# Performance work log

Measured on AMD Instinct MI355X. Metric: run time of the kernel, lower is better.

## Reference

```python
import jax, jax.numpy as jnp
import numpy as np

PAD = 32
NCLS = 33  # background + 32 instances
EPS = 1e-6


def lovasz_hinge_flat(logits, labels):
    # logits, labels: flat [P]; labels in {0,1} float
    signs = 2.0 * labels - 1.0
    errors = 1.0 - logits * signs
    perm = jnp.argsort(-errors)  # descending
    errors_sorted = errors[perm]
    gt_sorted = labels[perm]
    gts = gt_sorted.sum()
    intersection = gts - jnp.cumsum(gt_sorted)
    union = gts + jnp.cumsum(1.0 - gt_sorted)
    jaccard = 1.0 - intersection / union
    grad = jnp.concatenate([jaccard[:1], jaccard[1:] - jaccard[:-1]])
    return jnp.dot(jax.nn.relu(errors_sorted), jax.lax.stop_gradient(grad))


def setup_inputs() -> dict:
    key = jax.random.key(0)
    k1, k2, k3, k4, k5, k6 = jax.random.split(key, 6)
    B, C, H, W = 2, 16, 192, 192
    return {
        "y_embeddings": jax.random.normal(k1, (B, C, H, W), dtype=jnp.float32),
        "y_true": jax.random.randint(k2, (B, H, W), 0, NCLS),
        "W1": jax.random.normal(k3, (C, 32), dtype=jnp.float32) * 0.25,
        "b1": jax.random.normal(k4, (32,), dtype=jnp.float32) * 0.1,
        "W2": jax.random.normal(k5, (32,), dtype=jnp.float32) * 0.25,
        "b2": jax.random.normal(k6, (1,), dtype=jnp.float32) * 0.1,
    }


def reference(y_embeddings, y_true, W1, b1, W2, b2):
    def per_image(emb, gt):
        # emb: [C,H,W]; gt: [H,W] int
        emb = jnp.pad(emb, ((0, 0), (PAD, PAD), (PAD, PAD)))
        gt = jnp.pad(gt, ((PAD, PAD), (PAD, PAD)))
        # one-hot instance masks (drop background class 0): [N,Hp,Wp]
        oh = jnp.moveaxis(jax.nn.one_hot(gt, NCLS, dtype=emb.dtype), -1, 0)[1:]
        counts = jax.lax.stop_gradient(oh.sum(axis=(1, 2)) + EPS)  # [N]
        centers = jax.lax.stop_gradient(
            jnp.einsum('nhw,chw->nc', oh, emb) / counts[:, None])  # [N,C]
        # broadcast offsets: [N,C,Hp,Wp]
        sims = (centers[:, :, None, None] - emb[None]) / 32.0
        sims = jnp.clip(sims, -2.0, 2.0)
        feats = jnp.moveaxis(sims, 1, -1)  # [N,Hp,Wp,C]
        h = jax.nn.relu(feats @ W1 + b1)  # [N,Hp,Wp,32]
        logits = h @ W2 + b2[0]  # [N,Hp,Wp]
        return lovasz_hinge_flat(logits.reshape(-1), oh.reshape(-1))

    losses = jax.vmap(per_image)(y_embeddings, y_true)
    return jnp.mean(losses)
```

## Files before the change

kernel.cpp:

```cpp
#include <hip/hip_runtime.h>

#define NBINS 1024
#define IMG_HW 36864
#define T 256
#define BLKPI 144
#define NINST 32
#define CCH 16
#define NH 32
#define PADW 28672
#define NB 2
#define EPSF 1e-6f
#define NACC (NINST * (CCH + 1))

typedef unsigned long long u64;
typedef long long i64;
typedef float f32x4 __attribute__((ext_vector_type(4)));

#define OFF_WG   0
#define OFF_CSUM 16384
#define OFF_MAXB 25088
#define OFF_META 26240

__global__ void __launch_bounds__(256)
k_zero(u64* __restrict__ csum, float* __restrict__ out) {
    int tid = threadIdx.x;
    for (int i = tid; i < NB * NACC; i += 256) csum[i] = 0ull;
    if (tid == 0) out[0] = 0.f;
}

__global__ void __launch_bounds__(T)
k_centers(const float* __restrict__ emb, const int* __restrict__ gt,
          u64* __restrict__ csum, float* __restrict__ maxblk,
          u64* __restrict__ wg) {
    int blk = blockIdx.x, b = blockIdx.y;
    int tid = threadIdx.x;
    __shared__ i64 acc[NACC];
    __shared__ float mred[T / 64];

    int pix = blk * T + tid;
    int gtv = gt[(size_t)b * IMG_HW + pix];
    const float* e = emb + (size_t)b * CCH * IMG_HW + pix;
    float ev[CCH];
    float me = 0.f;
#pragma unroll
    for (int c = 0; c < CCH; c++) {
        ev[c] = e[c * IMG_HW];
        me = fmaxf(me, fabsf(ev[c]));
    }

    for (int i = tid; i < NACC; i += T) acc[i] = 0;
    int gid = (b * BLKPI + blk) * T + tid;
    if (gid < NB * NBINS) wg[gid] = 0ull;
    __syncthreads();

    if (gtv > 0) {
        int n = gtv - 1;
#pragma unroll
        for (int c = 0; c < CCH; c++) {
            i64 fx = (i64)((double)ev[c] * 4294967296.0);
            atomicAdd((u64*)&acc[n * CCH + c], (u64)fx);
        }
        atomicAdd((u64*)&acc[NINST * CCH + n], 1ull);
    }
#pragma unroll
    for (int off = 32; off > 0; off >>= 1) me = fmaxf(me, __shfl_down(me, off, 64));
    if ((tid & 63) == 0) mred[tid >> 6] = me;
    __syncthreads();
    if (tid == 0) {
        float m = 0.f;
#pragma unroll
        for (int w = 0; w < T / 64; w++) m = fmaxf(m, mred[w]);
        maxblk[b * BLKPI + blk] = m;
    }
    u64* cb = csum + (size_t)b * NACC;
    for (int i = tid; i < NACC; i += T) {
        u64 v = (u64)acc[i];
        if (v) atomicAdd(&cb[i], v);
    }
}

__global__ void __launch_bounds__(T, 2)
k_hist(const float* __restrict__ emb, const int* __restrict__ gt,
       const float* __restrict__ W1, const float* __restrict__ b1,
       const float* __restrict__ W2, const float* __restrict__ b2,
       const u64* __restrict__ csum, const float* __restrict__ maxblk,
       float* __restrict__ meta, u64* __restrict__ wg) {
    __shared__ unsigned int hist[NBINS];
    __shared__ __align__(16) float q_s[NINST][NH];
    __shared__ float a_s[NINST][CCH];
    __shared__ float redf[T / 64], redm[T / 64];
    __shared__ float semax[NINST];
    __shared__ float scons[1];

    int pixblk = blockIdx.x, b = blockIdx.y;
    int tid = threadIdx.x;

    int pix = pixblk * T + tid;
    int gtv = gt[(size_t)b * IMG_HW + pix];
    const float* e = emb + (size_t)b * CCH * IMG_HW + pix;
    float u[CCH];
#pragma unroll
    for (int c = 0; c < CCH; c++) u[c] = e[c * IMG_HW];

    for (int i = tid; i < NBINS; i += T) hist[i] = 0u;

    const u64* cb = csum + (size_t)b * NACC;
    float a_own = 0.f;
#pragma unroll
    for (int i = tid; i < NINST * CCH; i += T) {
        int n = i >> 4;
        float cnt = (float)(i64)cb[NINST * CCH + n] + EPSF;
        float a = (float)((double)(i64)cb[i] * (1.0 / 4294967296.0)) / cnt * (1.f / 32.f);
        a_s[n][i & 15] = a;
        a_own = fmaxf(a_own, fabsf(a));
    }
    float me = (tid < BLKPI) ? maxblk[b * BLKPI + tid] : 0.f;
#pragma unroll
    for (int off = 32; off > 0; off >>= 1) {
        me = fmaxf(me, __shfl_down(me, off, 64));
        a_own = fmaxf(a_own, __shfl_down(a_own, off, 64));
    }
    if ((tid & 63) == 0) { redf[tid >> 6] = me; redm[tid >> 6] = a_own; }
    __syncthreads();

    float maxug = 0.f, maxa = 0.f;
#pragma unroll
    for (int w = 0; w < T / 64; w++) {
        maxug = fmaxf(maxug, redf[w]);
        maxa = fmaxf(maxa, redm[w]);
    }
    maxug *= (1.f / 32.f);
    float b2v = b2[0];

    {
        int n = tid >> 3, jg = tid & 7;
        float lo_sum = 0.f, hi_sum = 0.f;
#pragma unroll
        for (int jj = 0; jj < 4; jj++) {
            int j = jg * 4 + jj;
            float s = b1[j], smin = s, smax = s;
#pragma unroll
            for (int c = 0; c < CCH; c++) {
                float w = W1[c * NH + j];
                float av = a_s[n][c];
                float lo = fmaxf(av - maxug, -2.f);
                float hi = fminf(av + maxug, 2.f);
                s += av * w;
                if (w >= 0.f) { smin += lo * w; smax += hi * w; }
                else          { smin += hi * w; smax += lo * w; }
            }
            q_s[n][j] = s;
            float hlo = fmaxf(smin, 0.f), hhi = fmaxf(smax, 0.f);
            float w2 = W2[j];
            if (w2 >= 0.f) { lo_sum += hlo * w2; hi_sum += hhi * w2; }
            else           { lo_sum += hhi * w2; hi_sum += hlo * w2; }
        }
#pragma unroll
        for (int off = 4; off > 0; off >>= 1) {
            lo_sum += __shfl_down(lo_sum, off, 8);
            hi_sum += __shfl_down(hi_sum, off, 8);
        }
        if ((tid & 7) == 0)
            semax[n] = 1.f + fmaxf(b2v + hi_sum, -(b2v + lo_sum));
    }
    __syncthreads();
    if (tid < 32) {
        float mval = semax[tid];
#pragma unroll
        for (int off = 16; off > 0; off >>= 1) mval = fmaxf(mval, __shfl_down(mval, off, 32));
        if (tid == 0) {
            float sc = (float)NBINS / (mval + 1e-3f);
            scons[0] = sc;
            if (pixblk == 0) meta[b] = sc;
        }
    }
    if (pixblk == 0 && tid >= 64 && tid < 96) {
        float g = (float)(i64)cb[NINST * CCH + (tid - 64)];
#pragma unroll
        for (int off = 16; off > 0; off >>= 1) g += __shfl_down(g, off, 32);
        if (tid == 64) meta[4 + b] = g;
    }
    __syncthreads();
    float scale = scons[0];

    if (pixblk == 0 && tid < NINST) {
        int n = tid;
        float logit = b2v;
        for (int j = 0; j < NH; j++) {
            float s = b1[j];
#pragma unroll
            for (int c = 0; c < CCH; c++)
                s += fminf(fmaxf(a_s[n][c], -2.f), 2.f) * W1[c * NH + j];
            logit += fmaxf(s, 0.f) * W2[j];
        }
        float er = 1.f + logit;
        if (er > 0.f) {
            int bin = min((int)(er * scale), NBINS - 1);
            atomicAdd(&wg[(size_t)b * NBINS + bin], (u64)PADW);
        }
    }

    float maxu = 0.f;
#pragma unroll
    for (int c = 0; c < CCH; c++) {
        u[c] *= (1.f / 32.f);
        maxu = fmaxf(maxu, fabsf(u[c]));
    }

    if (maxu + maxa <= 2.f) {
        const f32x4 z4 = {0.f, 0.f, 0.f, 0.f};
        f32x4 v4[8];
#pragma unroll
        for (int jj = 0; jj < 8; jj++) v4[jj] = z4;
#pragma unroll
        for (int c = 0; c < CCH; c++) {
            const f32x4* w1r = reinterpret_cast<const f32x4*>(W1 + c * NH);
            float uc = u[c];
#pragma unroll
            for (int jj = 0; jj < 8; jj++) v4[jj] += uc * w1r[jj];
        }
        f32x4 w2v[8];
        {
            const f32x4* w2p = reinterpret_cast<const f32x4*>(W2);
#pragma unroll
            for (int jj = 0; jj < 8; jj++) w2v[jj] = w2p[jj];
        }
#pragma unroll 4
        for (int n = 0; n < NINST; n++) {
            const f32x4* qn = reinterpret_cast<const f32x4*>(&q_s[n][0]);
            f32x4 acc = z4;
#pragma unroll
            for (int jj = 0; jj < 8; jj++) {
                f32x4 t = qn[jj] - v4[jj];
                t[0] = fmaxf(t[0], 0.f);
                t[1] = fmaxf(t[1], 0.f);
                t[2] = fmaxf(t[2], 0.f);
                t[3] = fmaxf(t[3], 0.f);
                acc += t * w2v[jj];
            }
            float logit = b2v + ((acc[0] + acc[1]) + (acc[2] + acc[3]));
            unsigned int label = (gtv == n + 1) ? 1u : 0u;
            float er = label ? (1.f - logit) : (1.f + logit);
            if (er > 0.f) {
                int bin = min((int)(er * scale), NBINS - 1);
                atomicAdd(&hist[bin], 1u | (label << 16));
            }
        }
    } else {
        for (int n = 0; n < NINST; n++) {
            float logit = b2v;
            for (int j = 0; j < NH; j++) {
                float s = b1[j];
#pragma unroll
                for (int c = 0; c < CCH; c++) {
                    float f = fminf(fmaxf(a_s[n][c] - u[c], -2.f), 2.f);
                    s += f * W1[c * NH + j];
                }
                logit += fmaxf(s, 0.f) * W2[j];
            }
            unsigned int label = (gtv == n + 1) ? 1u : 0u;
            float er = label ? (1.f - logit) : (1.f + logit);
            if (er > 0.f) {
                int bin = min((int)(er * scale), NBINS - 1);
                atomicAdd(&hist[bin], 1u | (label << 16));
            }
        }
    }
    __syncthreads();
    {
        u64* wgb = wg + (size_t)b * NBINS;
        for (int i = tid; i < NBINS; i += T) {
            unsigned int h = hist[i];
            if (h) atomicAdd(&wgb[i], (u64)(h & 0xffffu) | ((u64)(h >> 16) << 32));
        }
    }
}

__global__ void __launch_bounds__(1024)
k_loss(const u64* __restrict__ wg, const float* __restrict__ meta,
       float* __restrict__ out) {
    int b = blockIdx.x;
    int tid = threadIdx.x;
    const u64* wgb = wg + (size_t)b * NBINS;
    double G = (double)meta[4 + b];
    double invscale = 1.0 / (double)meta[b];

    int bin = NBINS - 1 - tid;
    u64 tot = wgb[bin];
    u64 incl = tot;
    int lane = tid & 63, wid = tid >> 6;
#pragma unroll
    for (int off = 1; off < 64; off <<= 1) {
        u64 x = __shfl_up(incl, off, 64);
        if (lane >= off) incl += x;
    }
    __shared__ u64 wpart[16];
    __shared__ double dred[16];
    if (lane == 63) wpart[wid] = incl;
    __syncthreads();
    u64 woff = 0;
    for (int w = 0; w < wid; w++) woff += wpart[w];
    u64 excl = woff + incl - tot;
    unsigned int p = (unsigned int)(excl & 0xffffffffull);
    unsigned int cs = (unsigned int)(excl >> 32);

    double loss = 0.0;
    unsigned int w = (unsigned int)(tot & 0xffffffffull);
    unsigned int g = (unsigned int)(tot >> 32);
    if (G > 0.5 && w) {
        double Js = 1.0 - (G - (double)cs) / (G + (double)p - (double)cs);
        unsigned int pe = p + w, ce = cs + g;
        double Je = 1.0 - (G - (double)ce) / (G + (double)pe - (double)ce);
        double rep = ((double)bin + 0.5) * invscale;
        loss = rep * (Je - Js);
    }
#pragma unroll
    for (int off = 32; off > 0; off >>= 1) loss += __shfl_down(loss, off, 64);
    if (lane == 0) dred[wid] = loss;
    __syncthreads();
    if (tid == 0) {
        double t = 0;
        for (int ww = 0; ww < 16; ww++) t += dred[ww];
        atomicAdd(out, (float)(t * 0.5));
    }
}

extern "C" void kernel_launch(void* const* d_in, const int* in_sizes, int n_in,
                              void* d_out, int out_size, void* d_ws, size_t ws_size,
                              hipStream_t stream) {
    const float* emb = (const float*)d_in[0];
    const int* gt = (const int*)d_in[1];
    const float* W1 = (const float*)d_in[2];
    const float* b1 = (const float*)d_in[3];
    const float* W2 = (const float*)d_in[4];
    const float* b2 = (const float*)d_in[5];
    float* out = (float*)d_out;
    char* ws = (char*)d_ws;

    u64* wg = (u64*)(ws + OFF_WG);
    u64* csum = (u64*)(ws + OFF_CSUM);
    float* maxblk = (float*)(ws + OFF_MAXB);
    float* meta = (float*)(ws + OFF_META);

    k_zero<<<dim3(1), 256, 0, stream>>>(csum, out);
    k_centers<<<dim3(BLKPI, NB), T, 0, stream>>>(emb, gt, csum, maxblk, wg);
    k_hist<<<dim3(BLKPI, NB), T, 0, stream>>>(emb, gt, W1, b1, W2, b2,
                                              csum, maxblk, meta, wg);
    k_loss<<<dim3(NB), 1024, 0, stream>>>(wg, meta, out);
}
```

Measured before the change: 39.36 us.

## Write pixel-major embedding copy in centers pass and use single-block loss reduction

k_centers now also writes each pixel's 16 channels as four contiguous float4s into a workspace buffer, and k_hist reads them with vector loads instead of 16 strided channel-plane loads. k_loss runs as a single block that loops over both images and writes the output directly, so the float atomic and the output zeroing in k_zero are no longer needed. The trade is an extra ~4.7 MB of writes in k_centers and fewer loss-kernel blocks against possibly cheaper loads in k_hist.

Result: slower. 41.57 us (+5.6%).

```diff
diff --git a/kernel.cpp b/kernel.cpp
--- a/kernel.cpp
+++ b/kernel.cpp
@@ -20,18 +20,18 @@
 #define OFF_CSUM 16384
 #define OFF_MAXB 25088
 #define OFF_META 26240
+#define OFF_EMBT 65536
 
 __global__ void __launch_bounds__(256)
-k_zero(u64* __restrict__ csum, float* __restrict__ out) {
+k_zero(u64* __restrict__ csum) {
     int tid = threadIdx.x;
     for (int i = tid; i < NB * NACC; i += 256) csum[i] = 0ull;
-    if (tid == 0) out[0] = 0.f;
 }
 
 __global__ void __launch_bounds__(T)
 k_centers(const float* __restrict__ emb, const int* __restrict__ gt,
           u64* __restrict__ csum, float* __restrict__ maxblk,
-          u64* __restrict__ wg) {
+          u64* __restrict__ wg, f32x4* __restrict__ embT) {
     int blk = blockIdx.x, b = blockIdx.y;
     int tid = threadIdx.x;
     __shared__ i64 acc[NACC];
@@ -53,6 +53,15 @@
     if (gid < NB * NBINS) wg[gid] = 0ull;
     __syncthreads();
 
+    {
+        f32x4* et = embT + (size_t)(b * IMG_HW + pix) * 4;
+#pragma unroll
+        for (int v = 0; v < 4; v++) {
+            f32x4 t = {ev[v * 4 + 0], ev[v * 4 + 1], ev[v * 4 + 2], ev[v * 4 + 3]};
+            et[v] = t;
+        }
+    }
+
     if (gtv > 0) {
         int n = gtv - 1;
 #pragma unroll
@@ -80,7 +89,7 @@
 }
 
 __global__ void __launch_bounds__(T, 2)
-k_hist(const float* __restrict__ emb, const int* __restrict__ gt,
+k_hist(const f32x4* __restrict__ embT, const int* __restrict__ gt,
        const float* __restrict__ W1, const float* __restrict__ b1,
        const float* __restrict__ W2, const float* __restrict__ b2,
        const u64* __restrict__ csum, const float* __restrict__ maxblk,
@@ -97,10 +106,10 @@
 
     int pix = pixblk * T + tid;
     int gtv = gt[(size_t)b * IMG_HW + pix];
-    const float* e = emb + (size_t)b * CCH * IMG_HW + pix;
-    float u[CCH];
-#pragma unroll
-    for (int c = 0; c < CCH; c++) u[c] = e[c * IMG_HW];
+    const f32x4* et = embT + (size_t)(b * IMG_HW + pix) * 4;
+    f32x4 u4[4];
+#pragma unroll
+    for (int v = 0; v < 4; v++) u4[v] = et[v];
 
     for (int i = tid; i < NBINS; i += T) hist[i] = 0u;
 
@@ -200,10 +209,11 @@
         }
     }
 
+    float u[CCH];
     float maxu = 0.f;
 #pragma unroll
     for (int c = 0; c < CCH; c++) {
-        u[c] *= (1.f / 32.f);
+        u[c] = u4[c >> 2][c & 3] * (1.f / 32.f);
         maxu = fmaxf(maxu, fabsf(u[c]));
     }
 
@@ -279,50 +289,55 @@
 __global__ void __launch_bounds__(1024)
 k_loss(const u64* __restrict__ wg, const float* __restrict__ meta,
        float* __restrict__ out) {
-    int b = blockIdx.x;
     int tid = threadIdx.x;
-    const u64* wgb = wg + (size_t)b * NBINS;
-    double G = (double)meta[4 + b];
-    double invscale = 1.0 / (double)meta[b];
-
-    int bin = NBINS - 1 - tid;
-    u64 tot = wgb[bin];
-    u64 incl = tot;
-    int lane = tid & 63, wid = tid >> 6;
-#pragma unroll
-    for (int off = 1; off < 64; off <<= 1) {
-        u64 x = __shfl_up(incl, off, 64);
-        if (lane >= off) incl += x;
-    }
     __shared__ u64 wpart[16];
     __shared__ double dred[16];
-    if (lane == 63) wpart[wid] = incl;
-    __syncthreads();
-    u64 woff = 0;
-    for (int w = 0; w < wid; w++) woff += wpart[w];
-    u64 excl = woff + incl - tot;
-    unsigned int p = (unsigned int)(excl & 0xffffffffull);
-    unsigned int cs = (unsigned int)(excl >> 32);
-
-    double loss = 0.0;
-    unsigned int w = (unsigned int)(tot & 0xffffffffull);
-    unsigned int g = (unsigned int)(tot >> 32);
-    if (G > 0.5 && w) {
-        double Js = 1.0 - (G - (double)cs) / (G + (double)p - (double)cs);
-        unsigned int pe = p + w, ce = cs + g;
-        double Je = 1.0 - (G - (double)ce) / (G + (double)pe - (double)ce);
-        double rep = ((double)bin + 0.5) * invscale;
-        loss = rep * (Je - Js);
-    }
-#pragma unroll
-    for (int off = 32; off > 0; off >>= 1) loss += __shfl_down(loss, off, 64);
-    if (lane == 0) dred[wid] = loss;
-    __syncthreads();
-    if (tid == 0) {
-        double t = 0;
-        for (int ww = 0; ww < 16; ww++) t += dred[ww];
-        atomicAdd(out, (float)(t * 0.5));
-    }
+    int lane = tid & 63, wid = tid >> 6;
+    double total = 0.0;
+
+    for (int b = 0; b < NB; b++) {
+        const u64* wgb = wg + (size_t)b * NBINS;
+        double G = (double)meta[4 + b];
+        double invscale = 1.0 / (double)meta[b];
+
+        int bin = NBINS - 1 - tid;
+        u64 tot = wgb[bin];
+        u64 incl = tot;
+#pragma unroll
+        for (int off = 1; off < 64; off <<= 1) {
+            u64 x = __shfl_up(incl, off, 64);
+            if (lane >= off) incl += x;
+        }
+        if (lane == 63) wpart[wid] = incl;
+        __syncthreads();
+        u64 woff = 0;
+        for (int w = 0; w < wid; w++) woff += wpart[w];
+        u64 excl = woff + incl - tot;
+        unsigned int p = (unsigned int)(excl & 0xffffffffull);
+        unsigned int cs = (unsigned int)(excl >> 32);
+
+        double loss = 0.0;
+        unsigned int w = (unsigned int)(tot & 0xffffffffull);
+        unsigned int g = (unsigned int)(tot >> 32);
+        if (G > 0.5 && w) {
+            double Js = 1.0 - (G - (double)cs) / (G + (double)p - (double)cs);
+            unsigned int pe = p + w, ce = cs + g;
+            double Je = 1.0 - (G - (double)ce) / (G + (double)pe - (double)ce);
+            double rep = ((double)bin + 0.5) * invscale;
+            loss = rep * (Je - Js);
+        }
+#pragma unroll
+        for (int off = 32; off > 0; off >>= 1) loss += __shfl_down(loss, off, 64);
+        if (lane == 0) dred[wid] = loss;
+        __syncthreads();
+        if (tid == 0) {
+            double t = 0;
+            for (int ww = 0; ww < 16; ww++) t += dred[ww];
+            total += t;
+        }
+        __syncthreads();
+    }
+    if (tid == 0) out[0] = (float)(total * 0.5);
 }
 
 extern "C" void kernel_launch(void* const* d_in, const int* in_sizes, int n_in,
@@ -341,10 +356,11 @@
     u64* csum = (u64*)(ws + OFF_CSUM);
     float* maxblk = (float*)(ws + OFF_MAXB);
     float* meta = (float*)(ws + OFF_META);
-
-    k_zero<<<dim3(1), 256, 0, stream>>>(csum, out);
-    k_centers<<<dim3(BLKPI, NB), T, 0, stream>>>(emb, gt, csum, maxblk, wg);
-    k_hist<<<dim3(BLKPI, NB), T, 0, stream>>>(emb, gt, W1, b1, W2, b2,
+    f32x4* embT = (f32x4*)(ws + OFF_EMBT);
+
+    k_zero<<<dim3(1), 256, 0, stream>>>(csum);
+    k_centers<<<dim3(BLKPI, NB), T, 0, stream>>>(emb, gt, csum, maxblk, wg, embT);
+    k_hist<<<dim3(BLKPI, NB), T, 0, stream>>>(embT, gt, W1, b1, W2, b2,
                                               csum, maxblk, meta, wg);
-    k_loss<<<dim3(NB), 1024, 0, stream>>>(wg, meta, out);
-}
+    k_loss<<<dim3(1), 1024, 0, stream>>>(wg, meta, out);
+}
```
